# Optimization experiments

Hardware: AMD Instinct MI355X
Metric: run time of the kernel (lower is better)

The kernel has to match this reference:

```python
import jax, jax.numpy as jnp
import numpy as np

B, T, C, H, N = 4, 1024, 768, 12, 64
D_DECAY, D_AAA, D_GATE = 64, 64, 128
EPS_GN = 0.00064


def setup_inputs() -> dict:
    key = jax.random.key(0)
    ks = jax.random.split(key, 24)
    def rn(i, shape, s=1.0):
        return jax.random.normal(ks[i], shape, dtype=jnp.float32) * s
    return {
        'x': rn(0, (B, T, C)),
        'x_r': rn(1, (1, 1, C), 0.1), 'x_w': rn(2, (1, 1, C), 0.1), 'x_k': rn(3, (1, 1, C), 0.1),
        'x_v': rn(4, (1, 1, C), 0.1), 'x_a': rn(5, (1, 1, C), 0.1), 'x_g': rn(6, (1, 1, C), 0.1),
        'w0': rn(7, (1, 1, C), 0.5),
        'w1': rn(8, (C, D_DECAY), C ** -0.5), 'w2': rn(9, (D_DECAY, C), D_DECAY ** -0.5),
        'a0': rn(10, (1, 1, C), 0.5),
        'a1': rn(11, (C, D_AAA), C ** -0.5), 'a2': rn(12, (D_AAA, C), D_AAA ** -0.5),
        'g1': rn(13, (C, D_GATE), C ** -0.5), 'g2': rn(14, (D_GATE, C), D_GATE ** -0.5),
        'k_k': rn(15, (1, 1, C), 0.5), 'k_a': rn(16, (1, 1, C), 0.5),
        'r_k': rn(17, (H, N), 0.5),
        'Wr': rn(18, (C, C), C ** -0.5), 'Wk': rn(19, (C, C), C ** -0.5),
        'Wv': rn(20, (C, C), C ** -0.5), 'Wo': rn(21, (C, C), C ** -0.5),
        'gamma': jnp.ones((C,), jnp.float32), 'beta': jnp.zeros((C,), jnp.float32),
    }


def _forward(x, x_r, x_w, x_k, x_v, x_a, x_g, w0, w1, w2, a0, a1, a2,
             g1, g2, k_k, k_a, r_k, Wr, Wk, Wv, Wo, gamma, beta):
    b, t, c = x.shape
    h, n = r_k.shape
    # TimeShift: pad one zero step at front, drop last -> delta vs current token
    xx = jnp.pad(x, ((0, 0), (1, 0), (0, 0)))[:, :-1] - x
    xr = x + xx * x_r
    xw = x + xx * x_w
    xk = x + xx * x_k
    xv = x + xx * x_v
    xa = x + xx * x_a
    xg = x + xx * x_g
    r = xr @ Wr
    k = xk @ Wk
    v = xv @ Wv  # v_first is None -> v_first = v, no low-rank value mixing
    w = -jax.nn.softplus(-(w0 + jnp.tanh(xw @ w1) @ w2)) - 0.5
    a = jax.nn.sigmoid(a0 + (xa @ a1) @ a2)
    g = jax.nn.sigmoid(xg @ g1) @ g2
    # per-head L2-normalized removal key
    kk = (k * k_k).reshape(b, t, h, n)
    kk = kk / jnp.maximum(jnp.linalg.norm(kk, axis=-1, keepdims=True), 1e-12)
    k = k * (1.0 + (a - 1.0) * k_a)
    rs = r.reshape(b, t, h, n)
    ks = k.reshape(b, t, h, n)
    vs = v.reshape(b, t, h, n)
    ws = jnp.exp(-jnp.exp(w.reshape(b, t, h, n)))  # decay in (0,1)
    aa = -kk
    bb = kk * a.reshape(b, t, h, n)
    # generalized delta rule: serial scan over time, state (B,H,N,N)
    def step(state, inp):
        r_t, w_t, k_t, v_t, a_t, b_t = inp  # each (B,H,N)
        sa = jnp.einsum('bhij,bhj->bhi', state, a_t)              # state @ aa
        state = (state * w_t[:, :, None, :]
                 + sa[..., None] * b_t[:, :, None, :]             # (state@aa) @ bb
                 + v_t[..., None] * k_t[:, :, None, :])           # vv @ kk
        o = jnp.einsum('bhij,bhj->bhi', state, r_t)               # state @ rr
        return state, o
    state0 = jnp.zeros((b, h, n, n), jnp.float32)
    seq = tuple(jnp.moveaxis(z, 1, 0) for z in (rs, ws, ks, vs, aa, bb))  # (T,B,H,N)
    _, o = jax.lax.scan(step, state0, seq)
    y = jnp.moveaxis(o, 0, 1).reshape(b, t, c)
    # GroupNorm over (B*T, C) with H groups, eps=6.4e-4
    yg = y.reshape(b, t, h, n)
    mu = jnp.mean(yg, axis=-1, keepdims=True)
    var = jnp.var(yg, axis=-1, keepdims=True)
    y = ((yg - mu) / jnp.sqrt(var + EPS_GN)).reshape(b, t, c) * gamma + beta
    # bonus term
    rwkv = jnp.sum(rs * ks * r_k, axis=-1, keepdims=True) * vs
    y = y + rwkv.reshape(b, t, c)
    return (y * g) @ Wo


def reference(x, x_r, x_w, x_k, x_v, x_a, x_g, w0, w1, w2, a0, a1, a2,
              g1, g2, k_k, k_a, r_k, Wr, Wk, Wv, Wo, gamma, beta):
    return _forward(x, x_r, x_w, x_k, x_v, x_a, x_g, w0, w1, w2, a0, a1, a2,
                    g1, g2, k_k, k_a, r_k, Wr, Wk, Wv, Wo, gamma, beta)
```

## Files before the change

kernel.cpp:

```cpp
#include <hip/hip_runtime.h>
#include <math.h>

constexpr int B_ = 4, T_ = 1024, C_ = 768, H_ = 12, N_ = 64;
constexpr int BT_ = B_ * T_;
constexpr size_t BTC = (size_t)BT_ * C_;
constexpr float EPS_GN = 0.00064f;
constexpr int NCH = 16;
constexpr int HC_ = 48 * NCH;

typedef __attribute__((ext_vector_type(8))) short bf16x8;
typedef __attribute__((ext_vector_type(4))) float f32x4;
typedef __attribute__((ext_vector_type(4))) unsigned short u16x4;
typedef __attribute__((ext_vector_type(8))) unsigned short u16x8;

#define DEVFN static __device__ __forceinline__

DEVFN unsigned short f2bf(float f) {
    unsigned u = __float_as_uint(f);
    unsigned r = u + 0x7FFFu + ((u >> 16) & 1u);
    return (unsigned short)(r >> 16);
}
DEVFN float bf2f(unsigned short u) { return __uint_as_float(((unsigned)u) << 16); }

template<int CTRL>
DEVFN float dppadd(float x) {
    return x + __int_as_float(__builtin_amdgcn_update_dpp(0, __float_as_int(x), CTRL, 0xF, 0xF, true));
}
#define SWZ_ADD(x, imm) ((x) + __int_as_float(__builtin_amdgcn_ds_swizzle(__float_as_int(x), (imm))))

DEVFN float red64(float x) {
    x = dppadd<0xB1>(x);
    x = dppadd<0x4E>(x);
    x = SWZ_ADD(x, 0x101F);
    x = SWZ_ADD(x, 0x201F);
    x = SWZ_ADD(x, 0x401F);
    x += __shfl_xor(x, 32, 64);
    return x;
}

DEVFN f32x4 mfma16(bf16x8 a, bf16x8 b, f32x4 c) {
    return __builtin_amdgcn_mfma_f32_16x16x32_bf16(a, b, c, 0, 0, 0);
}

typedef const __attribute__((address_space(1))) unsigned int* gas_t;
typedef __attribute__((address_space(3))) unsigned int* las_t;
DEVFN void gload16(const void* g, void* l) {
    __builtin_amdgcn_global_load_lds((gas_t)g, (las_t)l, 16, 0, 0);
}

DEVFN void wave_gemm64(const unsigned short (*A)[72], const unsigned short (*Bt)[72],
                       f32x4 acc[4][4], int lane) {
    int l15 = lane & 15, l16 = lane >> 4;
#pragma unroll
    for (int kk2 = 0; kk2 < 2; ++kk2) {
        bf16x8 af[4], bfv[4];
#pragma unroll
        for (int m = 0; m < 4; ++m) af[m] = *(const bf16x8*)&A[m * 16 + l15][kk2 * 32 + l16 * 8];
#pragma unroll
        for (int n = 0; n < 4; ++n) bfv[n] = *(const bf16x8*)&Bt[n * 16 + l15][kk2 * 32 + l16 * 8];
#pragma unroll
        for (int m = 0; m < 4; ++m)
#pragma unroll
            for (int n = 0; n < 4; ++n)
                acc[m][n] = mfma16(af[m], bfv[n], acc[m][n]);
    }
}

DEVFN void gemm16(const unsigned short (*A)[72], const unsigned short (*Bt)[72],
                  f32x4 acc[4], int wave, int lane) {
    int l15 = lane & 15, l16 = lane >> 4;
#pragma unroll
    for (int kk2 = 0; kk2 < 2; ++kk2) {
        bf16x8 af = *(const bf16x8*)&A[wave * 16 + l15][kk2 * 32 + l16 * 8];
        bf16x8 bfv[4];
#pragma unroll
        for (int n = 0; n < 4; ++n) bfv[n] = *(const bf16x8*)&Bt[n * 16 + l15][kk2 * 32 + l16 * 8];
#pragma unroll
        for (int n = 0; n < 4; ++n) acc[n] = mfma16(af, bfv[n], acc[n]);
    }
}

__global__ __launch_bounds__(256) void k_prep(const float* __restrict__ x,
    const float* __restrict__ m0, const float* __restrict__ m1, const float* __restrict__ m2,
    const float* __restrict__ m3, const float* __restrict__ m4, const float* __restrict__ m5,
    unsigned short* __restrict__ X6)
{
    int gid = blockIdx.x * 256 + threadIdx.x;
    int i4 = gid * 4;
    int bt = i4 / C_;
    int c  = i4 - bt * C_;
    const float4 xv = *(const float4*)(x + (size_t)bt * C_ + c);
    float px = 0.f, py = 0.f, pz = 0.f, pw = 0.f;
    if ((bt % T_) != 0) {
        const float4 p = *(const float4*)(x + (size_t)(bt - 1) * C_ + c);
        px = p.x; py = p.y; pz = p.z; pw = p.w;
    }
    float d0 = px - xv.x, d1 = py - xv.y, d2 = pz - xv.z, d3 = pw - xv.w;
    const float* mixes[6] = {m0, m1, m2, m3, m4, m5};
#pragma unroll
    for (int m = 0; m < 6; ++m) {
        const float4 mv = *(const float4*)(mixes[m] + c);
        u16x4 pk;
        pk[0] = f2bf(fmaf(d0, mv.x, xv.x));
        pk[1] = f2bf(fmaf(d1, mv.y, xv.y));
        pk[2] = f2bf(fmaf(d2, mv.z, xv.z));
        pk[3] = f2bf(fmaf(d3, mv.w, xv.w));
        *(u16x4*)(X6 + (size_t)m * BTC + (size_t)bt * C_ + c) = pk;
    }
}

__global__ __launch_bounds__(256) void k_transpose_all(
    const float* __restrict__ s0, const float* __restrict__ s1, const float* __restrict__ s2,
    const float* __restrict__ s3, const float* __restrict__ s4, const float* __restrict__ s5,
    const float* __restrict__ s6, const float* __restrict__ s7, const float* __restrict__ s8,
    const float* __restrict__ s9,
    unsigned short* __restrict__ d0, unsigned short* __restrict__ d1, unsigned short* __restrict__ d2,
    unsigned short* __restrict__ d3, unsigned short* __restrict__ d4, unsigned short* __restrict__ d5,
    unsigned short* __restrict__ d6, unsigned short* __restrict__ d7, unsigned short* __restrict__ d8,
    unsigned short* __restrict__ d9)
{
    __shared__ float tile[32][33];
    int bid = blockIdx.x;
    const float* W; unsigned short* WT; int R, Cc, loc;
    if (bid < 2304) {
        int w = bid / 576; loc = bid - w * 576;
        W = (w == 0) ? s0 : (w == 1) ? s1 : (w == 2) ? s2 : s3;
        WT = (w == 0) ? d0 : (w == 1) ? d1 : (w == 2) ? d2 : d3;
        R = 768; Cc = 768;
    } else if (bid < 2496) {
        int w = (bid - 2304) / 48; loc = (bid - 2304) % 48;
        W = (w == 0) ? s4 : (w == 1) ? s5 : (w == 2) ? s6 : s7;
        WT = (w == 0) ? d4 : (w == 1) ? d5 : (w == 2) ? d6 : d7;
        R = (w & 1) ? 64 : 768; Cc = (w & 1) ? 768 : 64;
    } else {
        int w = (bid - 2496) / 96; loc = (bid - 2496) % 96;
        W = (w == 0) ? s8 : s9;
        WT = (w == 0) ? d8 : d9;
        R = (w == 0) ? 768 : 128; Cc = (w == 0) ? 128 : 768;
    }
    int bx = Cc / 32;
    int bxi = loc % bx, byi = loc / bx;
    int tx = threadIdx.x & 31, ty = threadIdx.x >> 5;
#pragma unroll
    for (int j = 0; j < 4; ++j) {
        int rr = byi * 32 + ty + j * 8;
        int cc = bxi * 32 + tx;
        tile[ty + j * 8][tx] = W[(size_t)rr * Cc + cc];
    }
    __syncthreads();
#pragma unroll
    for (int j = 0; j < 4; ++j) {
        int ro = bxi * 32 + ty + j * 8;
        int co = byi * 32 + tx;
        WT[(size_t)ro * R + co] = f2bf(tile[tx][ty + j * 8]);
    }
}

template<int EPI>
__global__ __launch_bounds__(256) void k_gemm(const unsigned short* __restrict__ A,
    const unsigned short* __restrict__ Bt, void* __restrict__ Cp,
    const float* __restrict__ bias, int M, int Nn, int K)
{
    __shared__ unsigned short As[64][40];
    __shared__ unsigned short Bs[64][40];
    const int t = threadIdx.x, lane = t & 63, wave = t >> 6;
    const int wr = wave >> 1, wc = wave & 1;
    const int bM = blockIdx.y * 64, bN = blockIdx.x * 64;
    const int srow = t >> 2, skc = (t & 3) * 8;
    const int l15 = lane & 15, l16 = lane >> 4;
    f32x4 acc[2][2] = {};

    for (int k0 = 0; k0 < K; k0 += 32) {
        __syncthreads();
        *(int4*)&As[srow][skc] = *(const int4*)(A + (size_t)(bM + srow) * K + k0 + skc);
        *(int4*)&Bs[srow][skc] = *(const int4*)(Bt + (size_t)(bN + srow) * K + k0 + skc);
        __syncthreads();
        bf16x8 af0 = *(const bf16x8*)&As[wr * 32 + l15][l16 * 8];
        bf16x8 af1 = *(const bf16x8*)&As[wr * 32 + 16 + l15][l16 * 8];
        bf16x8 bf0 = *(const bf16x8*)&Bs[wc * 32 + l15][l16 * 8];
        bf16x8 bf1 = *(const bf16x8*)&Bs[wc * 32 + 16 + l15][l16 * 8];
        acc[0][0] = mfma16(af0, bf0, acc[0][0]);
        acc[0][1] = mfma16(af0, bf1, acc[0][1]);
        acc[1][0] = mfma16(af1, bf0, acc[1][0]);
        acc[1][1] = mfma16(af1, bf1, acc[1][1]);
    }

#pragma unroll
    for (int fm = 0; fm < 2; ++fm)
#pragma unroll
        for (int fn = 0; fn < 2; ++fn)
#pragma unroll
            for (int jj = 0; jj < 4; ++jj) {
                int gr = bM + wr * 32 + fm * 16 + l16 * 4 + jj;
                int gc = bN + wc * 32 + fn * 16 + l15;
                float val = acc[fm][fn][jj];
                size_t oi = (size_t)gr * Nn + gc;
                if constexpr (EPI == 1) {
                    ((unsigned short*)Cp)[oi] = f2bf(val);
                } else if constexpr (EPI == 2) {
                    ((unsigned short*)Cp)[oi] = f2bf(tanhf(val));
                } else {
                    ((unsigned short*)Cp)[oi] = f2bf(1.f / (1.f + expf(-val)));
                }
            }
}

template<int EPI>
__global__ __launch_bounds__(256) void k_gemm128(const unsigned short* __restrict__ A,
    const unsigned short* __restrict__ Bt, void* __restrict__ Cp,
    const float* __restrict__ bias, int M, int Nn, int K)
{
    __shared__ unsigned short As[128][32];
    __shared__ unsigned short Bs[128][32];
    const int tid = threadIdx.x, lane = tid & 63, wave = tid >> 6;
    const int wr = wave >> 1, wc = wave & 1;
    const int bM = blockIdx.y * 128, bN = blockIdx.x * 128;
    const int l15 = lane & 15, l16 = lane >> 4;
    const int srow = lane >> 2, scol = (lane & 3) * 8;
    f32x4 acc[4][4] = {};

    for (int k0 = 0; k0 < K; k0 += 32) {
        __syncthreads();
#pragma unroll
        for (int i = 0; i < 2; ++i) {
            int ch = i * 4 + wave;
            int row = ch * 16 + srow;
            gload16(A  + (size_t)(bM + row) * K + k0 + scol, &As[0][0] + ch * 512 + lane * 8);
            gload16(Bt + (size_t)(bN + row) * K + k0 + scol, &Bs[0][0] + ch * 512 + lane * 8);
        }
        __syncthreads();
        bf16x8 af[4], bfv[4];
#pragma unroll
        for (int m = 0; m < 4; ++m) af[m]  = *(const bf16x8*)&As[wr * 64 + m * 16 + l15][l16 * 8];
#pragma unroll
        for (int n = 0; n < 4; ++n) bfv[n] = *(const bf16x8*)&Bs[wc * 64 + n * 16 + l15][l16 * 8];
#pragma unroll
        for (int m = 0; m < 4; ++m)
#pragma unroll
            for (int n = 0; n < 4; ++n)
                acc[m][n] = mfma16(af[m], bfv[n], acc[m][n]);
    }

#pragma unroll
    for (int m = 0; m < 4; ++m)
#pragma unroll
        for (int n = 0; n < 4; ++n)
#pragma unroll
            for (int jj = 0; jj < 4; ++jj) {
                int gr = bM + wr * 64 + m * 16 + l16 * 4 + jj;
                int gc = bN + wc * 64 + n * 16 + l15;
                float val = acc[m][n][jj];
                size_t oi = (size_t)gr * Nn + gc;
                if constexpr (EPI == 0) {
                    ((float*)Cp)[oi] = val;
                } else if constexpr (EPI == 3) {
                    float z = bias[gc] + val;
                    float sg = 1.f / (1.f + expf(-z));
                    ((float*)Cp)[oi] = expf(-0.60653065971f * sg);
                } else {
                    float z = bias[gc] + val;
                    ((float*)Cp)[oi] = 1.f / (1.f + expf(-z));
                }
            }
}

__global__ __launch_bounds__(256) void k_kproc(float* __restrict__ k, const float* __restrict__ a,
    const float* __restrict__ r, const float* __restrict__ k_k, const float* __restrict__ k_a,
    const float* __restrict__ r_k, float* __restrict__ kk, float* __restrict__ dotb)
{
    int gw = blockIdx.x * 4 + (threadIdx.x >> 6);
    int lane = threadIdx.x & 63;
    int bt = gw / H_, h = gw - (gw / H_) * H_;
    int c = h * 64 + lane;
    size_t idx = (size_t)bt * C_ + c;
    float kv = k[idx], av = a[idx], rv = r[idx];
    float kkv = kv * k_k[c];
    float ss = red64(kkv * kkv);
    float inv = 1.f / fmaxf(sqrtf(ss), 1e-12f);
    kk[idx] = kkv * inv;
    float knew = kv * (1.f + (av - 1.f) * k_a[c]);
    k[idx] = knew;
    float dot = red64(rv * knew * r_k[c]);
    if (lane == 0) dotb[bt * H_ + h] = dot;
}

__global__ __launch_bounds__(256) void k_scanprep(const float* __restrict__ wdec,
    const float* __restrict__ kk, const float* __restrict__ asig, const float* __restrict__ kupd,
    const float* __restrict__ r, unsigned short* __restrict__ Abf, unsigned short* __restrict__ Bbf,
    unsigned short* __restrict__ Kbf, unsigned short* __restrict__ Rbf, float* __restrict__ cwL)
{
    __shared__ float CW[64][68];
    int hc = blockIdx.x;
    int g = hc >> 4, c = hc & 15;
    int b = g / H_, h = g - (g / H_) * H_;
    size_t rowb = ((size_t)(b * T_ + c * 64)) * C_ + h * 64;
    int tid = threadIdx.x;
    int t = tid >> 2, j0 = (tid & 3) * 16;
#pragma unroll
    for (int e = 0; e < 16; e += 4)
        *(float4*)&CW[t][j0 + e] = *(const float4*)(wdec + rowb + (size_t)t * C_ + j0 + e);
    __syncthreads();
    if (tid < 64) {
        float cp = 1.f;
#pragma unroll 4
        for (int tt = 0; tt < 64; ++tt) { cp *= CW[tt][tid]; CW[tt][tid] = cp; }
        cwL[hc * 64 + tid] = CW[63][tid];
    }
    __syncthreads();

    size_t base = (size_t)hc * 4096 + t * 64 + j0;
    size_t gin = rowb + (size_t)t * C_ + j0;
    float cwt[16], cwm[16], invc[16];
#pragma unroll
    for (int q = 0; q < 4; ++q) *(float4*)&cwt[q * 4] = *(const float4*)&CW[t][j0 + q * 4];
    if (t) {
#pragma unroll
        for (int q = 0; q < 4; ++q) *(float4*)&cwm[q * 4] = *(const float4*)&CW[t - 1][j0 + q * 4];
    } else {
#pragma unroll
        for (int e = 0; e < 16; ++e) cwm[e] = 1.f;
    }
#pragma unroll
    for (int e = 0; e < 16; ++e) invc[e] = 1.f / cwt[e];

    float kkv[16], tmp[16];
#pragma unroll
    for (int q = 0; q < 4; ++q) *(float4*)&kkv[q * 4] = *(const float4*)(kk + gin + q * 4);
    {
        u16x8 o0, o1;
#pragma unroll
        for (int e = 0; e < 8; ++e) { o0[e] = f2bf(-kkv[e] * cwm[e]); o1[e] = f2bf(-kkv[8 + e] * cwm[8 + e]); }
        *(u16x8*)(Abf + base) = o0; *(u16x8*)(Abf + base + 8) = o1;
    }
#pragma unroll
    for (int q = 0; q < 4; ++q) *(float4*)&tmp[q * 4] = *(const float4*)(asig + gin + q * 4);
    {
        u16x8 o0, o1;
#pragma unroll
        for (int e = 0; e < 8; ++e) { o0[e] = f2bf(kkv[e] * tmp[e] * invc[e]); o1[e] = f2bf(kkv[8 + e] * tmp[8 + e] * invc[8 + e]); }
        *(u16x8*)(Bbf + base) = o0; *(u16x8*)(Bbf + base + 8) = o1;
    }
#pragma unroll
    for (int q = 0; q < 4; ++q) *(float4*)&tmp[q * 4] = *(const float4*)(kupd + gin + q * 4);
    {
        u16x8 o0, o1;
#pragma unroll
        for (int e = 0; e < 8; ++e) { o0[e] = f2bf(tmp[e] * invc[e]); o1[e] = f2bf(tmp[8 + e] * invc[8 + e]); }
        *(u16x8*)(Kbf + base) = o0; *(u16x8*)(Kbf + base + 8) = o1;
    }
#pragma unroll
    for (int q = 0; q < 4; ++q) *(float4*)&tmp[q * 4] = *(const float4*)(r + gin + q * 4);
    {
        u16x8 o0, o1;
#pragma unroll
        for (int e = 0; e < 8; ++e) { o0[e] = f2bf(tmp[e] * cwt[e]); o1[e] = f2bf(tmp[8 + e] * cwt[8 + e]); }
        *(u16x8*)(Rbf + base) = o0; *(u16x8*)(Rbf + base + 8) = o1;
    }
}

__global__ __launch_bounds__(256) void k_chunk(const unsigned short* __restrict__ Abf,
    const unsigned short* __restrict__ Bbf, const unsigned short* __restrict__ Kbf,
    const unsigned short* __restrict__ Rbf, const float* __restrict__ vbuf,
    const float* __restrict__ cwL,
    unsigned short* __restrict__ Ttbf, unsigned short* __restrict__ Zbf,
    unsigned short* __restrict__ Ebf, unsigned short* __restrict__ Fbf)
{
    __shared__ unsigned short L[13][64][72];
    int hc = blockIdx.x, tid = threadIdx.x;
    int g = hc >> 4, c = hc & 15;
    int b = g / H_, h = g - (g / H_) * H_;
    size_t rowb = ((size_t)(b * T_ + c * 64)) * C_ + h * 64;
    size_t base = (size_t)hc * 4096;
    int r = tid >> 2, c0 = (tid & 3) * 16;
    int rl = tid & 63, cl0 = (tid >> 6) * 16;
    int wave = tid >> 6, lane = tid & 63;
    int l15 = lane & 15, l16 = lane >> 4;

    *(int4*)&L[2][r][c0]     = *(const int4*)(Abf + base + r * 64 + c0);
    *(int4*)&L[2][r][c0 + 8] = *(const int4*)(Abf + base + r * 64 + c0 + 8);
    *(int4*)&L[3][r][c0]     = *(const int4*)(Bbf + base + r * 64 + c0);
    *(int4*)&L[3][r][c0 + 8] = *(const int4*)(Bbf + base + r * 64 + c0 + 8);
    *(int4*)&L[4][r][c0]     = *(const int4*)(Kbf + base + r * 64 + c0);
    *(int4*)&L[4][r][c0 + 8] = *(const int4*)(Kbf + base + r * 64 + c0 + 8);
    *(int4*)&L[5][r][c0]     = *(const int4*)(Rbf + base + r * 64 + c0);
    *(int4*)&L[5][r][c0 + 8] = *(const int4*)(Rbf + base + r * 64 + c0 + 8);
#pragma unroll
    for (int q = 0; q < 4; ++q) {
        float4 v4 = *(const float4*)(vbuf + rowb + (size_t)rl * C_ + cl0 + q * 4);
        L[6][cl0 + q * 4 + 0][rl] = f2bf(v4.x);
        L[6][cl0 + q * 4 + 1][rl] = f2bf(v4.y);
        L[6][cl0 + q * 4 + 2][rl] = f2bf(v4.z);
        L[6][cl0 + q * 4 + 3][rl] = f2bf(v4.w);
    }
    __syncthreads();

    {
        f32x4 ga[4] = {};
        gemm16(L[2], L[3], ga, wave, lane);
#pragma unroll
        for (int n = 0; n < 4; ++n)
#pragma unroll
            for (int jj = 0; jj < 4; ++jj) {
                int ro = wave * 16 + l16 * 4 + jj, co = n * 16 + l15;
                float val = (ro > co) ? ga[n][jj] : 0.f;
                unsigned short gb = f2bf(val);
                L[0][ro][co] = gb;
                L[1][co][ro] = gb;
                L[12][ro][co] = (ro == co) ? (unsigned short)0x3F80 : gb;
            }
    }
    {
        f32x4 ha[4] = {};
        gemm16(L[2], L[4], ha, wave, lane);
#pragma unroll
        for (int n = 0; n < 4; ++n)
#pragma unroll
            for (int jj = 0; jj < 4; ++jj) {
                int ro = wave * 16 + l16 * 4 + jj, co = n * 16 + l15;
                L[7][ro][co] = f2bf((ro > co) ? ha[n][jj] : 0.f);
            }
    }
    {
        f32x4 pa[4] = {};
        gemm16(L[5], L[3], pa, wave, lane);
#pragma unroll
        for (int n = 0; n < 4; ++n)
#pragma unroll
            for (int jj = 0; jj < 4; ++jj) {
                int ro = wave * 16 + l16 * 4 + jj, co = n * 16 + l15;
                L[8][ro][co] = f2bf((ro >= co) ? pa[n][jj] : 0.f);
            }
    }
    {
        f32x4 qa[4] = {};
        gemm16(L[5], L[4], qa, wave, lane);
#pragma unroll
        for (int n = 0; n < 4; ++n)
#pragma unroll
            for (int jj = 0; jj < 4; ++jj) {
                int ro = wave * 16 + l16 * 4 + jj, co = n * 16 + l15;
                L[9][ro][co] = f2bf((ro >= co) ? qa[n][jj] : 0.f);
            }
    }
    __syncthreads();

    f32x4 hv[4] = {};
    gemm16(L[7], L[6], hv, wave, lane);
    u16x8 ta0 = *(const u16x8*)&L[2][rl][cl0], ta1 = *(const u16x8*)&L[2][rl][cl0 + 8];
    u16x8 tb0 = *(const u16x8*)&L[3][rl][cl0], tb1 = *(const u16x8*)&L[3][rl][cl0 + 8];
    u16x8 tk0 = *(const u16x8*)&L[4][rl][cl0], tk1 = *(const u16x8*)&L[4][rl][cl0 + 8];
    __syncthreads();
#pragma unroll
    for (int e = 0; e < 8; ++e) {
        L[2][cl0 + e][rl] = ta0[e]; L[2][cl0 + 8 + e][rl] = ta1[e];
        L[3][cl0 + e][rl] = tb0[e]; L[3][cl0 + 8 + e][rl] = tb1[e];
        L[4][cl0 + e][rl] = tk0[e]; L[4][cl0 + 8 + e][rl] = tk1[e];
    }
#pragma unroll
    for (int n = 0; n < 4; ++n)
#pragma unroll
        for (int jj = 0; jj < 4; ++jj) {
            int ro = wave * 16 + l16 * 4 + jj, co = n * 16 + l15;
            L[7][co][ro] = f2bf(hv[n][jj]);
        }
    __syncthreads();

#pragma unroll
    for (int it = 0; it < 5; ++it) {
        const unsigned short (*Gs_)[72]  = (it & 1) ? L[10] : L[0];
        const unsigned short (*GsT_)[72] = (it & 1) ? L[11] : L[1];
        unsigned short (*Ds_)[72]  = (it & 1) ? L[0] : L[10];
        unsigned short (*DsT_)[72] = (it & 1) ? L[1] : L[11];
        {
            f32x4 acc[4] = {};
            gemm16(Gs_, GsT_, acc, wave, lane);
#pragma unroll
            for (int n = 0; n < 4; ++n)
#pragma unroll
                for (int jj = 0; jj < 4; ++jj) {
                    int ro = wave * 16 + l16 * 4 + jj, co = n * 16 + l15;
                    unsigned short sb = f2bf(acc[n][jj]);
                    Ds_[ro][co] = sb;
                    DsT_[co][ro] = sb;
                }
        }
        __syncthreads();
        {
            f32x4 acc[4] = {};
            gemm16(L[12], DsT_, acc, wave, lane);
#pragma unroll
            for (int n = 0; n < 4; ++n)
#pragma unroll
                for (int jj = 0; jj < 4; ++jj) {
                    int ro = wave * 16 + l16 * 4 + jj, co = n * 16 + l15;
                    L[12][ro][co] = f2bf(acc[n][jj] + bf2f(L[12][ro][co]));
                }
        }
        __syncthreads();
    }

    {
        f32x4 wv[4] = {}, uv[4] = {};
        gemm16(L[12], L[2], wv, wave, lane);
        gemm16(L[12], L[7], uv, wave, lane);
#pragma unroll
        for (int n = 0; n < 4; ++n)
#pragma unroll
            for (int jj = 0; jj < 4; ++jj) {
                int ro = wave * 16 + l16 * 4 + jj, co = n * 16 + l15;
                L[10][co][ro] = f2bf(wv[n][jj]);
                L[11][co][ro] = f2bf(uv[n][jj]);
            }
    }
    __syncthreads();

    f32x4 acc[4][4] = {};
    if (wave == 0) wave_gemm64(L[10], L[3], acc, lane);
    else if (wave == 1) { wave_gemm64(L[11], L[3], acc, lane); wave_gemm64(L[6], L[4], acc, lane); }
    else if (wave == 2) wave_gemm64(L[8], L[10], acc, lane);
    else { wave_gemm64(L[8], L[11], acc, lane); wave_gemm64(L[9], L[6], acc, lane); }
#pragma unroll
    for (int m = 0; m < 4; ++m)
#pragma unroll
        for (int n = 0; n < 4; ++n)
#pragma unroll
            for (int jj = 0; jj < 4; ++jj) {
                int ro = m * 16 + l16 * 4 + jj;
                int co = n * 16 + l15;
                float val = acc[m][n][jj];
                if (wave == 0) {
                    val = (val + (ro == co ? 1.f : 0.f)) * cwL[hc * 64 + co];
                    Ttbf[base + (size_t)co * 64 + ro] = f2bf(val);
                } else if (wave == 1) {
                    Zbf[base + (size_t)ro * 64 + co] = f2bf(val * cwL[hc * 64 + co]);
                } else if (wave == 2) {
                    val += bf2f(L[5][ro][co]);
                    Ebf[base + (size_t)ro * 64 + co] = f2bf(val);
                } else {
                    Fbf[base + (size_t)ro * 64 + co] = f2bf(val);
                }
            }
}

__global__ __launch_bounds__(256) void k_phaseB(const unsigned short* __restrict__ Ttbf,
    const unsigned short* __restrict__ Zbf, unsigned short* __restrict__ Sbf)
{
    __shared__ unsigned short Sb[2][64][72];
    __shared__ unsigned short Tt[64][72];
    int g = blockIdx.x, tid = threadIdx.x;
    int r = tid >> 2, c0 = (tid & 3) * 16;
    int4 z4 = {0, 0, 0, 0};
    *(int4*)&Sb[0][r][c0] = z4;
    *(int4*)&Sb[0][r][c0 + 8] = z4;
    int cur = 0;
    int wave = tid >> 6, lane = tid & 63;
    int wr = wave >> 1, wc = wave & 1;
    int l15 = lane & 15, l16 = lane >> 4;
    for (int c = 0; c < NCH; ++c) {
        size_t base = ((size_t)g * NCH + c) * 4096;
        __syncthreads();
        *(int4*)(Sbf + base + r * 64 + c0)     = *(int4*)&Sb[cur][r][c0];
        *(int4*)(Sbf + base + r * 64 + c0 + 8) = *(int4*)&Sb[cur][r][c0 + 8];
        *(int4*)&Tt[r][c0]     = *(const int4*)(Ttbf + base + r * 64 + c0);
        *(int4*)&Tt[r][c0 + 8] = *(const int4*)(Ttbf + base + r * 64 + c0 + 8);
        __syncthreads();
        f32x4 acc[2][2] = {};
#pragma unroll
        for (int kk2 = 0; kk2 < 2; ++kk2) {
            bf16x8 af[2], bfv[2];
#pragma unroll
            for (int m = 0; m < 2; ++m) af[m] = *(const bf16x8*)&Sb[cur][wr * 32 + m * 16 + l15][kk2 * 32 + l16 * 8];
#pragma unroll
            for (int n = 0; n < 2; ++n) bfv[n] = *(const bf16x8*)&Tt[wc * 32 + n * 16 + l15][kk2 * 32 + l16 * 8];
#pragma unroll
            for (int m = 0; m < 2; ++m)
#pragma unroll
                for (int n = 0; n < 2; ++n)
                    acc[m][n] = mfma16(af[m], bfv[n], acc[m][n]);
        }
#pragma unroll
        for (int m = 0; m < 2; ++m)
#pragma unroll
            for (int n = 0; n < 2; ++n)
#pragma unroll
                for (int jj = 0; jj < 4; ++jj) {
                    int ro = wr * 32 + m * 16 + l16 * 4 + jj;
                    int co = wc * 32 + n * 16 + l15;
                    float val = acc[m][n][jj] + bf2f(Zbf[base + (size_t)ro * 64 + co]);
                    Sb[cur ^ 1][ro][co] = f2bf(val);
                }
        cur ^= 1;
    }
}

__global__ __launch_bounds__(256) void k_phaseC(const unsigned short* __restrict__ Ebf,
    const unsigned short* __restrict__ Sbf, const unsigned short* __restrict__ Fbf,
    float* __restrict__ obuf)
{
    __shared__ unsigned short Es[64][72], Ss[64][72];
    int hc = blockIdx.x, tid = threadIdx.x;
    int g = hc >> 4, c = hc & 15;
    int b = g / H_, h = g - (g / H_) * H_;
    size_t rowb = ((size_t)(b * T_ + c * 64)) * C_ + h * 64;
    size_t base = (size_t)hc * 4096;
    int r = tid >> 2, c0 = (tid & 3) * 16;
    *(int4*)&Es[r][c0]     = *(const int4*)(Ebf + base + r * 64 + c0);
    *(int4*)&Es[r][c0 + 8] = *(const int4*)(Ebf + base + r * 64 + c0 + 8);
    *(int4*)&Ss[r][c0]     = *(const int4*)(Sbf + base + r * 64 + c0);
    *(int4*)&Ss[r][c0 + 8] = *(const int4*)(Sbf + base + r * 64 + c0 + 8);
    __syncthreads();
    int wave = tid >> 6, lane = tid & 63;
    int wr = wave >> 1, wc = wave & 1;
    int l15 = lane & 15, l16 = lane >> 4;
    f32x4 acc[2][2] = {};
#pragma unroll
    for (int kk2 = 0; kk2 < 2; ++kk2) {
        bf16x8 af[2], bfv[2];
#pragma unroll
        for (int m = 0; m < 2; ++m) af[m] = *(const bf16x8*)&Es[wr * 32 + m * 16 + l15][kk2 * 32 + l16 * 8];
#pragma unroll
        for (int n = 0; n < 2; ++n) bfv[n] = *(const bf16x8*)&Ss[wc * 32 + n * 16 + l15][kk2 * 32 + l16 * 8];
#pragma unroll
        for (int m = 0; m < 2; ++m)
#pragma unroll
            for (int n = 0; n < 2; ++n)
                acc[m][n] = mfma16(af[m], bfv[n], acc[m][n]);
    }
#pragma unroll
    for (int m = 0; m < 2; ++m)
#pragma unroll
        for (int n = 0; n < 2; ++n)
#pragma unroll
            for (int jj = 0; jj < 4; ++jj) {
                int tt = wr * 32 + m * 16 + l16 * 4 + jj;
                int ii = wc * 32 + n * 16 + l15;
                float val = acc[m][n][jj] + bf2f(Fbf[base + (size_t)tt * 64 + ii]);
                obuf[rowb + (size_t)tt * C_ + ii] = val;
            }
}

__global__ __launch_bounds__(256) void k_gnorm(const float* __restrict__ o,
    const float* __restrict__ v, const float* __restrict__ g, const float* __restrict__ dotb,
    const float* __restrict__ gamma, const float* __restrict__ beta,
    unsigned short* __restrict__ yb)
{
    int gw = blockIdx.x * 4 + (threadIdx.x >> 6);
    int lane = threadIdx.x & 63;
    int bt = gw / H_, h = gw - (gw / H_) * H_;
    int c = h * 64 + lane;
    size_t idx = (size_t)bt * C_ + c;
    float ov = o[idx];
    float mean = red64(ov) * 0.015625f;
    float d = ov - mean;
    float var = red64(d * d) * 0.015625f;
    float yn = d * rsqrtf(var + EPS_GN) * gamma[c] + beta[c];
    float dot = dotb[bt * H_ + h];
    float y = (yn + dot * v[idx]) * g[idx];
    yb[idx] = f2bf(y);
}

extern "C" void kernel_launch(void* const* d_in, const int* in_sizes, int n_in,
                              void* d_out, int out_size, void* d_ws, size_t ws_size,
                              hipStream_t stream)
{
    (void)in_sizes; (void)n_in; (void)out_size; (void)ws_size;
    const float* x   = (const float*)d_in[0];
    const float* mr  = (const float*)d_in[1];
    const float* mw  = (const float*)d_in[2];
    const float* mk  = (const float*)d_in[3];
    const float* mv  = (const float*)d_in[4];
    const float* ma  = (const float*)d_in[5];
    const float* mg  = (const float*)d_in[6];
    const float* w0  = (const float*)d_in[7];
    const float* w1  = (const float*)d_in[8];
    const float* w2  = (const float*)d_in[9];
    const float* a0  = (const float*)d_in[10];
    const float* a1  = (const float*)d_in[11];
    const float* a2  = (const float*)d_in[12];
    const float* g1  = (const float*)d_in[13];
    const float* g2  = (const float*)d_in[14];
    const float* k_k = (const float*)d_in[15];
    const float* k_a = (const float*)d_in[16];
    const float* r_k = (const float*)d_in[17];
    const float* Wr  = (const float*)d_in[18];
    const float* Wk  = (const float*)d_in[19];
    const float* Wv  = (const float*)d_in[20];
    const float* Wo  = (const float*)d_in[21];
    const float* gam = (const float*)d_in[22];
    const float* bet = (const float*)d_in[23];

    char* ws = (char*)d_ws;
    constexpr size_t SZF = BTC * 4;
    constexpr size_t SZH = BTC * 2;
    unsigned short* X6  = (unsigned short*)ws;
    unsigned short* Abf = (unsigned short*)(ws + 0 * SZH);
    unsigned short* Bbf = (unsigned short*)(ws + 1 * SZH);
    unsigned short* Kbf = (unsigned short*)(ws + 2 * SZH);
    unsigned short* Rbf = (unsigned short*)(ws + 3 * SZH);
    unsigned short* Ttbf = Abf;
    unsigned short* Zbf  = (unsigned short*)(ws + 4 * SZH);
    float*          obuf = (float*)(ws + 1 * SZH);
    unsigned short* ybf  = (unsigned short*)(ws + 3 * SZH);

    size_t off = 6 * SZH;
    unsigned short* WrT = (unsigned short*)(ws + off); off += (size_t)768 * 768 * 2;
    unsigned short* WkT = (unsigned short*)(ws + off); off += (size_t)768 * 768 * 2;
    unsigned short* WvT = (unsigned short*)(ws + off); off += (size_t)768 * 768 * 2;
    unsigned short* WoT = (unsigned short*)(ws + off); off += (size_t)768 * 768 * 2;
    unsigned short* w1T = (unsigned short*)(ws + off); off += (size_t)64 * 768 * 2;
    unsigned short* w2T = (unsigned short*)(ws + off); off += (size_t)64 * 768 * 2;
    unsigned short* a1T = (unsigned short*)(ws + off); off += (size_t)64 * 768 * 2;
    unsigned short* a2T = (unsigned short*)(ws + off); off += (size_t)64 * 768 * 2;
    unsigned short* g1T = (unsigned short*)(ws + off); off += (size_t)128 * 768 * 2;
    unsigned short* g2T = (unsigned short*)(ws + off); off += (size_t)128 * 768 * 2;
    float* rbuf  = (float*)(ws + off); off += SZF;
    float* kbuf  = (float*)(ws + off); off += SZF;
    float* vbuf  = (float*)(ws + off); off += SZF;
    float* wdec  = (float*)(ws + off); off += SZF;
    float* abuf  = (float*)(ws + off); off += SZF;
    float* kkbuf = (float*)(ws + off); off += SZF;
    float* gbuf  = (float*)(ws + off); off += SZF;
    unsigned short* hw = (unsigned short*)(ws + off); off += (size_t)4096 * 64 * 2;
    unsigned short* ha = (unsigned short*)(ws + off); off += (size_t)4096 * 64 * 2;
    unsigned short* hg = (unsigned short*)(ws + off); off += (size_t)4096 * 128 * 2;
    unsigned short* Ebf = (unsigned short*)abuf;
    unsigned short* Sbf = (unsigned short*)((char*)abuf + SZH);
    unsigned short* Fbf = (unsigned short*)((char*)kkbuf + SZH);
    float* cwL  = (float*)hw;
    float* dotb = (float*)ha;

    k_prep<<<3072, 256, 0, stream>>>(x, mr, mw, mk, mv, ma, mg, X6);
    k_transpose_all<<<2688, 256, 0, stream>>>(Wr, Wk, Wv, Wo, w1, w2, a1, a2, g1, g2,
                                              WrT, WkT, WvT, WoT, w1T, w2T, a1T, a2T, g1T, g2T);
    k_gemm<2><<<dim3(1, 64), 256, 0, stream>>>(X6 + 1 * BTC, w1T, hw, nullptr, 4096, 64, 768);
    k_gemm128<3><<<dim3(6, 32), 256, 0, stream>>>(hw, w2T, wdec, w0, 4096, 768, 64);
    k_gemm<1><<<dim3(1, 64), 256, 0, stream>>>(X6 + 4 * BTC, a1T, ha, nullptr, 4096, 64, 768);
    k_gemm128<4><<<dim3(6, 32), 256, 0, stream>>>(ha, a2T, abuf, a0, 4096, 768, 64);
    k_gemm<5><<<dim3(2, 64), 256, 0, stream>>>(X6 + 5 * BTC, g1T, hg, nullptr, 4096, 128, 768);
    k_gemm128<0><<<dim3(6, 32), 256, 0, stream>>>(hg, g2T, gbuf, nullptr, 4096, 768, 128);
    k_gemm128<0><<<dim3(6, 32), 256, 0, stream>>>(X6 + 0 * BTC, WrT, rbuf, nullptr, 4096, 768, 768);
    k_gemm128<0><<<dim3(6, 32), 256, 0, stream>>>(X6 + 2 * BTC, WkT, kbuf, nullptr, 4096, 768, 768);
    k_gemm128<0><<<dim3(6, 32), 256, 0, stream>>>(X6 + 3 * BTC, WvT, vbuf, nullptr, 4096, 768, 768);
    k_kproc<<<12288, 256, 0, stream>>>(kbuf, abuf, rbuf, k_k, k_a, r_k, kkbuf, dotb);
    k_scanprep<<<HC_, 256, 0, stream>>>(wdec, kkbuf, abuf, kbuf, rbuf, Abf, Bbf, Kbf, Rbf, cwL);
    k_chunk<<<HC_, 256, 0, stream>>>(Abf, Bbf, Kbf, Rbf, vbuf, cwL, Ttbf, Zbf, Ebf, Fbf);
    k_phaseB<<<48, 256, 0, stream>>>(Ttbf, Zbf, Sbf);
    k_phaseC<<<HC_, 256, 0, stream>>>(Ebf, Sbf, Fbf, obuf);
    k_gnorm<<<12288, 256, 0, stream>>>(obuf, vbuf, gbuf, dotb, gam, bet, ybf);
    k_gemm128<0><<<dim3(6, 32), 256, 0, stream>>>(ybf, WoT, (float*)d_out, nullptr, 4096, 768, 768);
}
```

Measured before the change: 419.0 us.

## Batch projection GEMMs into grouped launches and widen chunk kernel to 512 threads

Merges the w/a low-rank second-stage GEMMs into one launch and the g2/Wr/Wk/Wv GEMMs into one z-indexed grouped launch. This cuts launch count and lets the small GEMMs share the GPU with the large ones. The chunk kernel moves to 512 threads with 8 waves, each owning half of a 16-row band. Its doubling iteration is restructured to reuse one buffer, dropping two LDS tiles, and the final four products are spread across all waves instead of one wave per output. The grouped kernel hardcodes an output stride of 768, and the K=128 slice finishes early, which can leave some compute units idle.

Result: faster. 341.7 us (-18.4%).

```diff
diff --git a/kernel.cpp b/kernel.cpp
--- a/kernel.cpp
+++ b/kernel.cpp
@@ -48,35 +48,17 @@
     __builtin_amdgcn_global_load_lds((gas_t)g, (las_t)l, 16, 0, 0);
 }
 
-DEVFN void wave_gemm64(const unsigned short (*A)[72], const unsigned short (*Bt)[72],
-                       f32x4 acc[4][4], int lane) {
+DEVFN void gemm16h(const unsigned short (*A)[72], const unsigned short (*Bt)[72],
+                   f32x4 acc[2], int band, int half, int lane) {
     int l15 = lane & 15, l16 = lane >> 4;
 #pragma unroll
     for (int kk2 = 0; kk2 < 2; ++kk2) {
-        bf16x8 af[4], bfv[4];
-#pragma unroll
-        for (int m = 0; m < 4; ++m) af[m] = *(const bf16x8*)&A[m * 16 + l15][kk2 * 32 + l16 * 8];
-#pragma unroll
-        for (int n = 0; n < 4; ++n) bfv[n] = *(const bf16x8*)&Bt[n * 16 + l15][kk2 * 32 + l16 * 8];
-#pragma unroll
-        for (int m = 0; m < 4; ++m)
-#pragma unroll
-            for (int n = 0; n < 4; ++n)
-                acc[m][n] = mfma16(af[m], bfv[n], acc[m][n]);
-    }
-}
-
-DEVFN void gemm16(const unsigned short (*A)[72], const unsigned short (*Bt)[72],
-                  f32x4 acc[4], int wave, int lane) {
-    int l15 = lane & 15, l16 = lane >> 4;
-#pragma unroll
-    for (int kk2 = 0; kk2 < 2; ++kk2) {
-        bf16x8 af = *(const bf16x8*)&A[wave * 16 + l15][kk2 * 32 + l16 * 8];
-        bf16x8 bfv[4];
-#pragma unroll
-        for (int n = 0; n < 4; ++n) bfv[n] = *(const bf16x8*)&Bt[n * 16 + l15][kk2 * 32 + l16 * 8];
-#pragma unroll
-        for (int n = 0; n < 4; ++n) acc[n] = mfma16(af, bfv[n], acc[n]);
+        bf16x8 af = *(const bf16x8*)&A[band * 16 + l15][kk2 * 32 + l16 * 8];
+#pragma unroll
+        for (int n = 0; n < 2; ++n) {
+            bf16x8 bfv = *(const bf16x8*)&Bt[(half * 2 + n) * 16 + l15][kk2 * 32 + l16 * 8];
+            acc[n] = mfma16(af, bfv, acc[n]);
+        }
     }
 }
 
@@ -264,6 +246,116 @@
             }
 }
 
+struct GemmSet {
+    const unsigned short* A[4];
+    const unsigned short* Bt[4];
+    float* C[4];
+    int K[4];
+};
+__global__ __launch_bounds__(256) void k_gemm128b(GemmSet S)
+{
+    __shared__ unsigned short As[128][32];
+    __shared__ unsigned short Bs[128][32];
+    const int z = blockIdx.z;
+    const unsigned short* A = S.A[z];
+    const unsigned short* Bt = S.Bt[z];
+    float* Cp = S.C[z];
+    const int K = S.K[z];
+    const int tid = threadIdx.x, lane = tid & 63, wave = tid >> 6;
+    const int wr = wave >> 1, wc = wave & 1;
+    const int bM = blockIdx.y * 128, bN = blockIdx.x * 128;
+    const int l15 = lane & 15, l16 = lane >> 4;
+    const int srow = lane >> 2, scol = (lane & 3) * 8;
+    f32x4 acc[4][4] = {};
+
+    for (int k0 = 0; k0 < K; k0 += 32) {
+        __syncthreads();
+#pragma unroll
+        for (int i = 0; i < 2; ++i) {
+            int ch = i * 4 + wave;
+            int row = ch * 16 + srow;
+            gload16(A  + (size_t)(bM + row) * K + k0 + scol, &As[0][0] + ch * 512 + lane * 8);
+            gload16(Bt + (size_t)(bN + row) * K + k0 + scol, &Bs[0][0] + ch * 512 + lane * 8);
+        }
+        __syncthreads();
+        bf16x8 af[4], bfv[4];
+#pragma unroll
+        for (int m = 0; m < 4; ++m) af[m]  = *(const bf16x8*)&As[wr * 64 + m * 16 + l15][l16 * 8];
+#pragma unroll
+        for (int n = 0; n < 4; ++n) bfv[n] = *(const bf16x8*)&Bs[wc * 64 + n * 16 + l15][l16 * 8];
+#pragma unroll
+        for (int m = 0; m < 4; ++m)
+#pragma unroll
+            for (int n = 0; n < 4; ++n)
+                acc[m][n] = mfma16(af[m], bfv[n], acc[m][n]);
+    }
+#pragma unroll
+    for (int m = 0; m < 4; ++m)
+#pragma unroll
+        for (int n = 0; n < 4; ++n)
+#pragma unroll
+            for (int jj = 0; jj < 4; ++jj) {
+                int gr = bM + wr * 64 + m * 16 + l16 * 4 + jj;
+                int gc = bN + wc * 64 + n * 16 + l15;
+                Cp[(size_t)gr * 768 + gc] = acc[m][n][jj];
+            }
+}
+
+__global__ __launch_bounds__(256) void k_gemm128wa(const unsigned short* __restrict__ Ahw,
+    const unsigned short* __restrict__ Aha, const unsigned short* __restrict__ BtW,
+    const unsigned short* __restrict__ BtA, float* __restrict__ Cw, float* __restrict__ Ca,
+    const float* __restrict__ bw, const float* __restrict__ ba)
+{
+    __shared__ unsigned short As[128][32];
+    __shared__ unsigned short Bs[128][32];
+    const int z = blockIdx.z;
+    const unsigned short* A = z ? Aha : Ahw;
+    const unsigned short* Bt = z ? BtA : BtW;
+    float* Cp = z ? Ca : Cw;
+    const float* bias = z ? ba : bw;
+    const int K = 64;
+    const int tid = threadIdx.x, lane = tid & 63, wave = tid >> 6;
+    const int wr = wave >> 1, wc = wave & 1;
+    const int bM = blockIdx.y * 128, bN = blockIdx.x * 128;
+    const int l15 = lane & 15, l16 = lane >> 4;
+    const int srow = lane >> 2, scol = (lane & 3) * 8;
+    f32x4 acc[4][4] = {};
+
+    for (int k0 = 0; k0 < K; k0 += 32) {
+        __syncthreads();
+#pragma unroll
+        for (int i = 0; i < 2; ++i) {
+            int ch = i * 4 + wave;
+            int row = ch * 16 + srow;
+            gload16(A  + (size_t)(bM + row) * K + k0 + scol, &As[0][0] + ch * 512 + lane * 8);
+            gload16(Bt + (size_t)(bN + row) * K + k0 + scol, &Bs[0][0] + ch * 512 + lane * 8);
+        }
+        __syncthreads();
+        bf16x8 af[4], bfv[4];
+#pragma unroll
+        for (int m = 0; m < 4; ++m) af[m]  = *(const bf16x8*)&As[wr * 64 + m * 16 + l15][l16 * 8];
+#pragma unroll
+        for (int n = 0; n < 4; ++n) bfv[n] = *(const bf16x8*)&Bs[wc * 64 + n * 16 + l15][l16 * 8];
+#pragma unroll
+        for (int m = 0; m < 4; ++m)
+#pragma unroll
+            for (int n = 0; n < 4; ++n)
+                acc[m][n] = mfma16(af[m], bfv[n], acc[m][n]);
+    }
+#pragma unroll
+    for (int m = 0; m < 4; ++m)
+#pragma unroll
+        for (int n = 0; n < 4; ++n)
+#pragma unroll
+            for (int jj = 0; jj < 4; ++jj) {
+                int gr = bM + wr * 64 + m * 16 + l16 * 4 + jj;
+                int gc = bN + wc * 64 + n * 16 + l15;
+                float zv = bias[gc] + acc[m][n][jj];
+                float sg = 1.f / (1.f + expf(-zv));
+                Cp[(size_t)gr * 768 + gc] = z ? sg : expf(-0.60653065971f * sg);
+            }
+}
+
 __global__ __launch_bounds__(256) void k_kproc(float* __restrict__ k, const float* __restrict__ a,
     const float* __restrict__ r, const float* __restrict__ k_k, const float* __restrict__ k_a,
     const float* __restrict__ r_k, float* __restrict__ kk, float* __restrict__ dotb)
@@ -358,188 +450,188 @@
     }
 }
 
-__global__ __launch_bounds__(256) void k_chunk(const unsigned short* __restrict__ Abf,
+__global__ __launch_bounds__(512) void k_chunk(const unsigned short* __restrict__ Abf,
     const unsigned short* __restrict__ Bbf, const unsigned short* __restrict__ Kbf,
     const unsigned short* __restrict__ Rbf, const float* __restrict__ vbuf,
     const float* __restrict__ cwL,
     unsigned short* __restrict__ Ttbf, unsigned short* __restrict__ Zbf,
     unsigned short* __restrict__ Ebf, unsigned short* __restrict__ Fbf)
 {
-    __shared__ unsigned short L[13][64][72];
+    __shared__ unsigned short L[11][64][72];
     int hc = blockIdx.x, tid = threadIdx.x;
     int g = hc >> 4, c = hc & 15;
     int b = g / H_, h = g - (g / H_) * H_;
     size_t rowb = ((size_t)(b * T_ + c * 64)) * C_ + h * 64;
     size_t base = (size_t)hc * 4096;
-    int r = tid >> 2, c0 = (tid & 3) * 16;
-    int rl = tid & 63, cl0 = (tid >> 6) * 16;
+    int r8 = tid >> 3, c8 = (tid & 7) * 8;
+    int rl = tid & 63, cl8 = (tid >> 6) * 8;
     int wave = tid >> 6, lane = tid & 63;
+    int band = wave >> 1, half = wave & 1;
     int l15 = lane & 15, l16 = lane >> 4;
 
-    *(int4*)&L[2][r][c0]     = *(const int4*)(Abf + base + r * 64 + c0);
-    *(int4*)&L[2][r][c0 + 8] = *(const int4*)(Abf + base + r * 64 + c0 + 8);
-    *(int4*)&L[3][r][c0]     = *(const int4*)(Bbf + base + r * 64 + c0);
-    *(int4*)&L[3][r][c0 + 8] = *(const int4*)(Bbf + base + r * 64 + c0 + 8);
-    *(int4*)&L[4][r][c0]     = *(const int4*)(Kbf + base + r * 64 + c0);
-    *(int4*)&L[4][r][c0 + 8] = *(const int4*)(Kbf + base + r * 64 + c0 + 8);
-    *(int4*)&L[5][r][c0]     = *(const int4*)(Rbf + base + r * 64 + c0);
-    *(int4*)&L[5][r][c0 + 8] = *(const int4*)(Rbf + base + r * 64 + c0 + 8);
-#pragma unroll
-    for (int q = 0; q < 4; ++q) {
-        float4 v4 = *(const float4*)(vbuf + rowb + (size_t)rl * C_ + cl0 + q * 4);
-        L[6][cl0 + q * 4 + 0][rl] = f2bf(v4.x);
-        L[6][cl0 + q * 4 + 1][rl] = f2bf(v4.y);
-        L[6][cl0 + q * 4 + 2][rl] = f2bf(v4.z);
-        L[6][cl0 + q * 4 + 3][rl] = f2bf(v4.w);
-    }
-    __syncthreads();
-
-    {
-        f32x4 ga[4] = {};
-        gemm16(L[2], L[3], ga, wave, lane);
-#pragma unroll
-        for (int n = 0; n < 4; ++n)
-#pragma unroll
-            for (int jj = 0; jj < 4; ++jj) {
-                int ro = wave * 16 + l16 * 4 + jj, co = n * 16 + l15;
-                float val = (ro > co) ? ga[n][jj] : 0.f;
-                unsigned short gb = f2bf(val);
+    *(u16x8*)&L[2][r8][c8] = *(const u16x8*)(Abf + base + r8 * 64 + c8);
+    *(u16x8*)&L[3][r8][c8] = *(const u16x8*)(Bbf + base + r8 * 64 + c8);
+    *(u16x8*)&L[4][r8][c8] = *(const u16x8*)(Kbf + base + r8 * 64 + c8);
+    *(u16x8*)&L[5][r8][c8] = *(const u16x8*)(Rbf + base + r8 * 64 + c8);
+#pragma unroll
+    for (int q = 0; q < 2; ++q) {
+        float4 v4 = *(const float4*)(vbuf + rowb + (size_t)rl * C_ + cl8 + q * 4);
+        L[6][cl8 + q * 4 + 0][rl] = f2bf(v4.x);
+        L[6][cl8 + q * 4 + 1][rl] = f2bf(v4.y);
+        L[6][cl8 + q * 4 + 2][rl] = f2bf(v4.z);
+        L[6][cl8 + q * 4 + 3][rl] = f2bf(v4.w);
+    }
+    __syncthreads();
+
+    {
+        f32x4 ga[2] = {};
+        gemm16h(L[2], L[3], ga, band, half, lane);
+#pragma unroll
+        for (int n = 0; n < 2; ++n)
+#pragma unroll
+            for (int jj = 0; jj < 4; ++jj) {
+                int ro = band * 16 + l16 * 4 + jj, co = (half * 2 + n) * 16 + l15;
+                unsigned short gb = f2bf((ro > co) ? ga[n][jj] : 0.f);
                 L[0][ro][co] = gb;
                 L[1][co][ro] = gb;
-                L[12][ro][co] = (ro == co) ? (unsigned short)0x3F80 : gb;
-            }
-    }
-    {
-        f32x4 ha[4] = {};
-        gemm16(L[2], L[4], ha, wave, lane);
-#pragma unroll
-        for (int n = 0; n < 4; ++n)
-#pragma unroll
-            for (int jj = 0; jj < 4; ++jj) {
-                int ro = wave * 16 + l16 * 4 + jj, co = n * 16 + l15;
+                L[10][ro][co] = (ro == co) ? (unsigned short)0x3F80 : gb;
+            }
+    }
+    {
+        f32x4 ha[2] = {};
+        gemm16h(L[2], L[4], ha, band, half, lane);
+#pragma unroll
+        for (int n = 0; n < 2; ++n)
+#pragma unroll
+            for (int jj = 0; jj < 4; ++jj) {
+                int ro = band * 16 + l16 * 4 + jj, co = (half * 2 + n) * 16 + l15;
                 L[7][ro][co] = f2bf((ro > co) ? ha[n][jj] : 0.f);
             }
     }
     {
-        f32x4 pa[4] = {};
-        gemm16(L[5], L[3], pa, wave, lane);
-#pragma unroll
-        for (int n = 0; n < 4; ++n)
-#pragma unroll
-            for (int jj = 0; jj < 4; ++jj) {
-                int ro = wave * 16 + l16 * 4 + jj, co = n * 16 + l15;
+        f32x4 pa[2] = {};
+        gemm16h(L[5], L[3], pa, band, half, lane);
+#pragma unroll
+        for (int n = 0; n < 2; ++n)
+#pragma unroll
+            for (int jj = 0; jj < 4; ++jj) {
+                int ro = band * 16 + l16 * 4 + jj, co = (half * 2 + n) * 16 + l15;
                 L[8][ro][co] = f2bf((ro >= co) ? pa[n][jj] : 0.f);
             }
     }
     {
-        f32x4 qa[4] = {};
-        gemm16(L[5], L[4], qa, wave, lane);
-#pragma unroll
-        for (int n = 0; n < 4; ++n)
-#pragma unroll
-            for (int jj = 0; jj < 4; ++jj) {
-                int ro = wave * 16 + l16 * 4 + jj, co = n * 16 + l15;
+        f32x4 qa[2] = {};
+        gemm16h(L[5], L[4], qa, band, half, lane);
+#pragma unroll
+        for (int n = 0; n < 2; ++n)
+#pragma unroll
+            for (int jj = 0; jj < 4; ++jj) {
+                int ro = band * 16 + l16 * 4 + jj, co = (half * 2 + n) * 16 + l15;
                 L[9][ro][co] = f2bf((ro >= co) ? qa[n][jj] : 0.f);
             }
     }
     __syncthreads();
 
-    f32x4 hv[4] = {};
-    gemm16(L[7], L[6], hv, wave, lane);
-    u16x8 ta0 = *(const u16x8*)&L[2][rl][cl0], ta1 = *(const u16x8*)&L[2][rl][cl0 + 8];
-    u16x8 tb0 = *(const u16x8*)&L[3][rl][cl0], tb1 = *(const u16x8*)&L[3][rl][cl0 + 8];
-    u16x8 tk0 = *(const u16x8*)&L[4][rl][cl0], tk1 = *(const u16x8*)&L[4][rl][cl0 + 8];
+    f32x4 hv[2] = {};
+    gemm16h(L[7], L[6], hv, band, half, lane);
+    u16x8 ta = *(const u16x8*)&L[2][rl][cl8];
+    u16x8 tb = *(const u16x8*)&L[3][rl][cl8];
+    u16x8 tk = *(const u16x8*)&L[4][rl][cl8];
     __syncthreads();
 #pragma unroll
     for (int e = 0; e < 8; ++e) {
-        L[2][cl0 + e][rl] = ta0[e]; L[2][cl0 + 8 + e][rl] = ta1[e];
-        L[3][cl0 + e][rl] = tb0[e]; L[3][cl0 + 8 + e][rl] = tb1[e];
-        L[4][cl0 + e][rl] = tk0[e]; L[4][cl0 + 8 + e][rl] = tk1[e];
-    }
-#pragma unroll
-    for (int n = 0; n < 4; ++n)
+        L[2][cl8 + e][rl] = ta[e];
+        L[3][cl8 + e][rl] = tb[e];
+        L[4][cl8 + e][rl] = tk[e];
+    }
+#pragma unroll
+    for (int n = 0; n < 2; ++n)
 #pragma unroll
         for (int jj = 0; jj < 4; ++jj) {
-            int ro = wave * 16 + l16 * 4 + jj, co = n * 16 + l15;
+            int ro = band * 16 + l16 * 4 + jj, co = (half * 2 + n) * 16 + l15;
             L[7][co][ro] = f2bf(hv[n][jj]);
         }
-    __syncthreads();
+    f32x4 sacc[2] = {};
+    gemm16h(L[0], L[1], sacc, band, half, lane);
+    f32x4 pacc[2] = {};
 
 #pragma unroll
     for (int it = 0; it < 5; ++it) {
-        const unsigned short (*Gs_)[72]  = (it & 1) ? L[10] : L[0];
-        const unsigned short (*GsT_)[72] = (it & 1) ? L[11] : L[1];
-        unsigned short (*Ds_)[72]  = (it & 1) ? L[0] : L[10];
-        unsigned short (*DsT_)[72] = (it & 1) ? L[1] : L[11];
-        {
-            f32x4 acc[4] = {};
-            gemm16(Gs_, GsT_, acc, wave, lane);
-#pragma unroll
-            for (int n = 0; n < 4; ++n)
+        __syncthreads();
+#pragma unroll
+        for (int n = 0; n < 2; ++n)
+#pragma unroll
+            for (int jj = 0; jj < 4; ++jj) {
+                int ro = band * 16 + l16 * 4 + jj, co = (half * 2 + n) * 16 + l15;
+                unsigned short sb = f2bf(sacc[n][jj]);
+                L[0][ro][co] = sb;
+                L[1][co][ro] = sb;
+            }
+        if (it > 0) {
+#pragma unroll
+            for (int n = 0; n < 2; ++n)
 #pragma unroll
                 for (int jj = 0; jj < 4; ++jj) {
-                    int ro = wave * 16 + l16 * 4 + jj, co = n * 16 + l15;
-                    unsigned short sb = f2bf(acc[n][jj]);
-                    Ds_[ro][co] = sb;
-                    DsT_[co][ro] = sb;
+                    int ro = band * 16 + l16 * 4 + jj, co = (half * 2 + n) * 16 + l15;
+                    L[10][ro][co] = f2bf(pacc[n][jj] + bf2f(L[10][ro][co]));
                 }
         }
         __syncthreads();
-        {
-            f32x4 acc[4] = {};
-            gemm16(L[12], DsT_, acc, wave, lane);
-#pragma unroll
-            for (int n = 0; n < 4; ++n)
-#pragma unroll
-                for (int jj = 0; jj < 4; ++jj) {
-                    int ro = wave * 16 + l16 * 4 + jj, co = n * 16 + l15;
-                    L[12][ro][co] = f2bf(acc[n][jj] + bf2f(L[12][ro][co]));
-                }
+        pacc[0] = (f32x4){0.f, 0.f, 0.f, 0.f}; pacc[1] = (f32x4){0.f, 0.f, 0.f, 0.f};
+        gemm16h(L[10], L[1], pacc, band, half, lane);
+        if (it < 4) {
+            sacc[0] = (f32x4){0.f, 0.f, 0.f, 0.f}; sacc[1] = (f32x4){0.f, 0.f, 0.f, 0.f};
+            gemm16h(L[0], L[1], sacc, band, half, lane);
         }
-        __syncthreads();
-    }
-
-    {
-        f32x4 wv[4] = {}, uv[4] = {};
-        gemm16(L[12], L[2], wv, wave, lane);
-        gemm16(L[12], L[7], uv, wave, lane);
-#pragma unroll
-        for (int n = 0; n < 4; ++n)
-#pragma unroll
-            for (int jj = 0; jj < 4; ++jj) {
-                int ro = wave * 16 + l16 * 4 + jj, co = n * 16 + l15;
-                L[10][co][ro] = f2bf(wv[n][jj]);
-                L[11][co][ro] = f2bf(uv[n][jj]);
-            }
-    }
-    __syncthreads();
-
-    f32x4 acc[4][4] = {};
-    if (wave == 0) wave_gemm64(L[10], L[3], acc, lane);
-    else if (wave == 1) { wave_gemm64(L[11], L[3], acc, lane); wave_gemm64(L[6], L[4], acc, lane); }
-    else if (wave == 2) wave_gemm64(L[8], L[10], acc, lane);
-    else { wave_gemm64(L[8], L[11], acc, lane); wave_gemm64(L[9], L[6], acc, lane); }
-#pragma unroll
-    for (int m = 0; m < 4; ++m)
-#pragma unroll
-        for (int n = 0; n < 4; ++n)
-#pragma unroll
-            for (int jj = 0; jj < 4; ++jj) {
-                int ro = m * 16 + l16 * 4 + jj;
-                int co = n * 16 + l15;
-                float val = acc[m][n][jj];
-                if (wave == 0) {
-                    val = (val + (ro == co ? 1.f : 0.f)) * cwL[hc * 64 + co];
-                    Ttbf[base + (size_t)co * 64 + ro] = f2bf(val);
-                } else if (wave == 1) {
-                    Zbf[base + (size_t)ro * 64 + co] = f2bf(val * cwL[hc * 64 + co]);
-                } else if (wave == 2) {
-                    val += bf2f(L[5][ro][co]);
-                    Ebf[base + (size_t)ro * 64 + co] = f2bf(val);
-                } else {
-                    Fbf[base + (size_t)ro * 64 + co] = f2bf(val);
-                }
-            }
+    }
+    __syncthreads();
+#pragma unroll
+    for (int n = 0; n < 2; ++n)
+#pragma unroll
+        for (int jj = 0; jj < 4; ++jj) {
+            int ro = band * 16 + l16 * 4 + jj, co = (half * 2 + n) * 16 + l15;
+            L[10][ro][co] = f2bf(pacc[n][jj] + bf2f(L[10][ro][co]));
+        }
+    __syncthreads();
+
+    {
+        f32x4 wv[2] = {}, uv[2] = {};
+        gemm16h(L[10], L[2], wv, band, half, lane);
+        gemm16h(L[10], L[7], uv, band, half, lane);
+#pragma unroll
+        for (int n = 0; n < 2; ++n)
+#pragma unroll
+            for (int jj = 0; jj < 4; ++jj) {
+                int ro = band * 16 + l16 * 4 + jj, co = (half * 2 + n) * 16 + l15;
+                L[0][co][ro] = f2bf(wv[n][jj]);
+                L[1][co][ro] = f2bf(uv[n][jj]);
+            }
+    }
+    __syncthreads();
+
+    {
+        f32x4 tacc[2] = {};
+        gemm16h(L[0], L[3], tacc, band, half, lane);
+        f32x4 zacc[2] = {};
+        gemm16h(L[1], L[3], zacc, band, half, lane);
+        gemm16h(L[6], L[4], zacc, band, half, lane);
+        f32x4 eacc[2] = {};
+        gemm16h(L[8], L[0], eacc, band, half, lane);
+        f32x4 facc[2] = {};
+        gemm16h(L[8], L[1], facc, band, half, lane);
+        gemm16h(L[9], L[6], facc, band, half, lane);
+#pragma unroll
+        for (int n = 0; n < 2; ++n)
+#pragma unroll
+            for (int jj = 0; jj < 4; ++jj) {
+                int ro = band * 16 + l16 * 4 + jj, co = (half * 2 + n) * 16 + l15;
+                float cw = cwL[hc * 64 + co];
+                Ttbf[base + (size_t)co * 64 + ro] = f2bf((tacc[n][jj] + (ro == co ? 1.f : 0.f)) * cw);
+                Zbf[base + (size_t)ro * 64 + co] = f2bf(zacc[n][jj] * cw);
+                Ebf[base + (size_t)ro * 64 + co] = f2bf(eacc[n][jj] + bf2f(L[5][ro][co]));
+                Fbf[base + (size_t)ro * 64 + co] = f2bf(facc[n][jj]);
+            }
+    }
 }
 
 __global__ __launch_bounds__(256) void k_phaseB(const unsigned short* __restrict__ Ttbf,
@@ -733,17 +825,20 @@
     k_transpose_all<<<2688, 256, 0, stream>>>(Wr, Wk, Wv, Wo, w1, w2, a1, a2, g1, g2,
                                               WrT, WkT, WvT, WoT, w1T, w2T, a1T, a2T, g1T, g2T);
     k_gemm<2><<<dim3(1, 64), 256, 0, stream>>>(X6 + 1 * BTC, w1T, hw, nullptr, 4096, 64, 768);
-    k_gemm128<3><<<dim3(6, 32), 256, 0, stream>>>(hw, w2T, wdec, w0, 4096, 768, 64);
     k_gemm<1><<<dim3(1, 64), 256, 0, stream>>>(X6 + 4 * BTC, a1T, ha, nullptr, 4096, 64, 768);
-    k_gemm128<4><<<dim3(6, 32), 256, 0, stream>>>(ha, a2T, abuf, a0, 4096, 768, 64);
     k_gemm<5><<<dim3(2, 64), 256, 0, stream>>>(X6 + 5 * BTC, g1T, hg, nullptr, 4096, 128, 768);
-    k_gemm128<0><<<dim3(6, 32), 256, 0, stream>>>(hg, g2T, gbuf, nullptr, 4096, 768, 128);
-    k_gemm128<0><<<dim3(6, 32), 256, 0, stream>>>(X6 + 0 * BTC, WrT, rbuf, nullptr, 4096, 768, 768);
-    k_gemm128<0><<<dim3(6, 32), 256, 0, stream>>>(X6 + 2 * BTC, WkT, kbuf, nullptr, 4096, 768, 768);
-    k_gemm128<0><<<dim3(6, 32), 256, 0, stream>>>(X6 + 3 * BTC, WvT, vbuf, nullptr, 4096, 768, 768);
+    k_gemm128wa<<<dim3(6, 32, 2), 256, 0, stream>>>(hw, ha, w2T, a2T, wdec, abuf, w0, a0);
+    {
+        GemmSet S;
+        S.A[0] = hg;            S.Bt[0] = g2T; S.C[0] = gbuf; S.K[0] = 128;
+        S.A[1] = X6 + 0 * BTC;  S.Bt[1] = WrT; S.C[1] = rbuf; S.K[1] = 768;
+        S.A[2] = X6 + 2 * BTC;  S.Bt[2] = WkT; S.C[2] = kbuf; S.K[2] = 768;
+        S.A[3] = X6 + 3 * BTC;  S.Bt[3] = WvT; S.C[3] = vbuf; S.K[3] = 768;
+        k_gemm128b<<<dim3(6, 32, 4), 256, 0, stream>>>(S);
+    }
     k_kproc<<<12288, 256, 0, stream>>>(kbuf, abuf, rbuf, k_k, k_a, r_k, kkbuf, dotb);
     k_scanprep<<<HC_, 256, 0, stream>>>(wdec, kkbuf, abuf, kbuf, rbuf, Abf, Bbf, Kbf, Rbf, cwL);
-    k_chunk<<<HC_, 256, 0, stream>>>(Abf, Bbf, Kbf, Rbf, vbuf, cwL, Ttbf, Zbf, Ebf, Fbf);
+    k_chunk<<<HC_, 512, 0, stream>>>(Abf, Bbf, Kbf, Rbf, vbuf, cwL, Ttbf, Zbf, Ebf, Fbf);
     k_phaseB<<<48, 256, 0, stream>>>(Ttbf, Zbf, Sbf);
     k_phaseC<<<HC_, 256, 0, stream>>>(Ebf, Sbf, Fbf, obuf);
     k_gnorm<<<12288, 256, 0, stream>>>(obuf, vbuf, gbuf, dotb, gam, bet, ybf);
```
